# Kernel tuning notes

Measured on AMD Instinct MI355X. Metric: run time of the kernel, lower is better.

Reference implementation:

```python
import jax, jax.numpy as jnp
import numpy as np

B, S, D = 1, 4096, 2048
H, KV, HD = 16, 4, 128
GROUPS = H // KV
SCALE = HD ** -0.5
ROPE_BASE = 10000.0
NEG = -1e9


def _rope_tables():
    inv_freq = 1.0 / (ROPE_BASE ** (jnp.arange(0, HD, 2, dtype=jnp.float32) / HD))  # [HD/2]
    pos = jnp.arange(S, dtype=jnp.float32)
    freqs = pos[:, None] * inv_freq[None, :]            # [S, HD/2]
    emb = jnp.concatenate([freqs, freqs], axis=-1)      # [S, HD] (HF convention)
    return jnp.cos(emb)[None], jnp.sin(emb)[None]       # [1, S, HD]


def setup_inputs() -> dict:
    key = jax.random.key(0)
    ks = jax.random.split(key, 6)
    cos, sin = _rope_tables()
    causal = jnp.tril(jnp.ones((S, S), dtype=bool))
    attention_mask = jnp.where(causal, 0.0, NEG).astype(jnp.float32)[None, None]  # [1,1,S,S]
    std = 0.02
    return {
        "hidden_states": jax.random.normal(ks[0], (B, S, D), jnp.float32),
        "cos": cos.astype(jnp.float32),
        "sin": sin.astype(jnp.float32),
        "attention_mask": attention_mask,
        "wq": jax.random.normal(ks[1], (H * HD, D), jnp.float32) * std,
        "wk": jax.random.normal(ks[2], (KV * HD, D), jnp.float32) * std,
        "wv": jax.random.normal(ks[3], (KV * HD, D), jnp.float32) * std,
        "wo": jax.random.normal(ks[4], (D, H * HD), jnp.float32) * std,
    }


def _rotate_half(x):
    x1, x2 = x[..., : HD // 2], x[..., HD // 2:]
    return jnp.concatenate([-x2, x1], axis=-1)


def reference(hidden_states, cos, sin, attention_mask, wq, wk, wv, wo):
    b, s, _ = hidden_states.shape
    # projections -> [B, n_heads, S, HD]
    q = (hidden_states @ wq.T).reshape(b, s, H, HD).transpose(0, 2, 1, 3)
    k = (hidden_states @ wk.T).reshape(b, s, KV, HD).transpose(0, 2, 1, 3)
    v = (hidden_states @ wv.T).reshape(b, s, KV, HD).transpose(0, 2, 1, 3)
    # RoPE (HF apply_rotary_pos_emb, unsqueeze head dim)
    c, sn = cos[:, None], sin[:, None]
    q = q * c + _rotate_half(q) * sn
    k = k * c + _rotate_half(k) * sn
    # GQA: repeat kv heads
    k = jnp.repeat(k, GROUPS, axis=1)
    v = jnp.repeat(v, GROUPS, axis=1)
    # eager attention
    scores = jnp.einsum("bhqd,bhkd->bhqk", q, k) * SCALE + attention_mask
    attn = jax.nn.softmax(scores, axis=-1)
    out = jnp.einsum("bhqk,bhkd->bhqd", attn, v)
    out = out.transpose(0, 2, 1, 3).reshape(b, s, H * HD)
    # output projection (all-reduce is identity at world_size=1)
    return out @ wo.T
```

## Files before the change

kernel.cpp:

```cpp
#include <hip/hip_runtime.h>
#include <hip/hip_bf16.h>

#define SEQ   4096
#define DMODEL 2048
#define NHEAD 16
#define NKVH  4
#define HDIM  128
#define NQ    (NHEAD*HDIM)
#define NKV   (NKVH*HDIM)
#define NQKV  (NQ + 2*NKV)
#define SCALE 0.08838834764831845f
#define LOG2E 1.4426950408889634f
#define SCL2  (SCALE * LOG2E)

typedef __bf16 bf16x4 __attribute__((ext_vector_type(4)));
typedef __bf16 bf16x8 __attribute__((ext_vector_type(8)));
typedef float  f32x4  __attribute__((ext_vector_type(4)));

#define GLOBAL_CPTR(x) ((const __attribute__((address_space(1))) void*)(x))
#define LDS_PTR(x)     ((__attribute__((address_space(3))) void*)(x))

__global__ __launch_bounds__(256)
void convert_kernel(__bf16* __restrict__ dst, const float* __restrict__ src, int n8)
{
    const int i = blockIdx.x * 256 + threadIdx.x;
    if (i >= n8) return;
    const size_t e0 = (size_t)i * 8;
    const float4 a = *(const float4*)(src + e0);
    const float4 b = *(const float4*)(src + e0 + 4);
    bf16x8 o;
    o[0]=(__bf16)a.x; o[1]=(__bf16)a.y; o[2]=(__bf16)a.z; o[3]=(__bf16)a.w;
    o[4]=(__bf16)b.x; o[5]=(__bf16)b.y; o[6]=(__bf16)b.z; o[7]=(__bf16)b.w;
    *(bf16x8*)(dst + e0) = o;
}

__global__ __launch_bounds__(256)
void gemm_bt(const __bf16* __restrict__ A, const __bf16* __restrict__ Bw,
             void* __restrict__ Cv, __bf16* __restrict__ kb2, __bf16* __restrict__ vt2,
             const float* __restrict__ ct, const float* __restrict__ st,
             int M, int N, int K, int cmode)
{
    __shared__ alignas(16) __bf16 As[2][128*32];
    __shared__ alignas(16) __bf16 Bs[2][128*32];

    const int tid  = threadIdx.x;
    const int w    = tid >> 6;
    const int lane = tid & 63;
    const int l16  = lane & 15;
    const int quad = lane >> 4;
    const int m0 = blockIdx.y * 128;
    const int n0 = blockIdx.x * 128;

    const int srow = lane >> 2;
    const int scol = (lane & 3) * 8;

    const int wm = (w >> 1) * 64;
    int coff[4];
    #pragma unroll
    for (int nt = 0; nt < 4; ++nt)
        coff[nt] = (cmode == 3) ? ((w & 1) * 32 + ((nt & 2) ? 64 : 0) + (nt & 1) * 16)
                                : ((w & 1) * 64 + nt * 16);

    f32x4 acc[4][4];
    #pragma unroll
    for (int mt = 0; mt < 4; ++mt)
        #pragma unroll
        for (int nt = 0; nt < 4; ++nt)
            acc[mt][nt] = (f32x4){0.f, 0.f, 0.f, 0.f};

    auto STAGE = [&](int k0, int b) {
        #pragma unroll
        for (int c = 0; c < 2; ++c) {
            const int r0 = w * 32 + c * 16;
            const __bf16* ga = A + (size_t)(m0 + r0 + srow) * K + k0 + scol;
            __builtin_amdgcn_global_load_lds(GLOBAL_CPTR(ga), LDS_PTR(&As[b][r0 * 32]), 16, 0, 0);
            const __bf16* gb = Bw + (size_t)(n0 + r0 + srow) * K + k0 + scol;
            __builtin_amdgcn_global_load_lds(GLOBAL_CPTR(gb), LDS_PTR(&Bs[b][r0 * 32]), 16, 0, 0);
        }
    };

    STAGE(0, 0);
    for (int k0 = 0; k0 < K; k0 += 32) {
        const int b = (k0 >> 5) & 1;
        __syncthreads();
        if (k0 + 32 < K) STAGE(k0 + 32, b ^ 1);

        bf16x8 af[4], bf[4];
        #pragma unroll
        for (int mt = 0; mt < 4; ++mt)
            af[mt] = *(const bf16x8*)&As[b][(wm + mt*16 + l16) * 32 + quad * 8];
        #pragma unroll
        for (int nt = 0; nt < 4; ++nt)
            bf[nt] = *(const bf16x8*)&Bs[b][(coff[nt] + l16) * 32 + quad * 8];
        __builtin_amdgcn_s_setprio(1);
        #pragma unroll
        for (int mt = 0; mt < 4; ++mt)
            #pragma unroll
            for (int nt = 0; nt < 4; ++nt)
                acc[mt][nt] = __builtin_amdgcn_mfma_f32_16x16x32_bf16(
                    af[mt], bf[nt], acc[mt][nt], 0, 0, 0);
        __builtin_amdgcn_s_setprio(0);
    }

    if (cmode == 3) {
        if (n0 >= 2560) {
            #pragma unroll
            for (int mt = 0; mt < 4; ++mt)
                #pragma unroll
                for (int nt = 0; nt < 4; ++nt) {
                    const int col = (n0 - 2560) + coff[nt] + l16;
                    const int row = m0 + wm + mt*16 + quad*4;
                    bf16x4 pk;
                    #pragma unroll
                    for (int r = 0; r < 4; ++r) pk[r] = (__bf16)acc[mt][nt][r];
                    *(bf16x4*)&vt2[(size_t)col * M + row] = pk;
                }
        } else {
            __bf16* dst;
            int ncols, cb;
            if (n0 < 2048) { dst = (__bf16*)Cv; ncols = NQ;  cb = n0; }
            else           { dst = kb2;         ncols = NKV; cb = n0 - 2048; }
            #pragma unroll
            for (int mt = 0; mt < 4; ++mt)
                #pragma unroll
                for (int np = 0; np < 2; ++np) {
                    const int d = coff[np] + l16;
                    #pragma unroll
                    for (int r = 0; r < 4; ++r) {
                        const int s = m0 + wm + mt*16 + quad*4 + r;
                        const float c  = ct[s * HDIM + d];
                        const float sn = st[s * HDIM + d];
                        const float x1 = acc[mt][np][r];
                        const float x2 = acc[mt][np + 2][r];
                        dst[(size_t)s * ncols + cb + d]      = (__bf16)(x1 * c - x2 * sn);
                        dst[(size_t)s * ncols + cb + d + 64] = (__bf16)(x2 * c + x1 * sn);
                    }
                }
        }
    } else if (cmode == 1) {
        float* Cf = (float*)Cv;
        #pragma unroll
        for (int mt = 0; mt < 4; ++mt)
            #pragma unroll
            for (int nt = 0; nt < 4; ++nt) {
                const int row = m0 + wm + mt*16 + quad*4;
                const int col = n0 + coff[nt] + l16;
                #pragma unroll
                for (int r = 0; r < 4; ++r)
                    Cf[(size_t)(row + r) * N + col] = acc[mt][nt][r];
            }
    } else {
        __bf16* Cb = (__bf16*)Cv;
        #pragma unroll
        for (int mt = 0; mt < 4; ++mt)
            #pragma unroll
            for (int nt = 0; nt < 4; ++nt) {
                const int row = m0 + wm + mt*16 + quad*4;
                const int col = n0 + coff[nt] + l16;
                #pragma unroll
                for (int r = 0; r < 4; ++r)
                    Cb[(size_t)(row + r) * N + col] = (__bf16)acc[mt][nt][r];
            }
    }
}

__global__ __launch_bounds__(512, 4)
void attn_kernel(__bf16* __restrict__ QO, const __bf16* __restrict__ Kb,
                 const __bf16* __restrict__ Vt)
{
    __shared__ alignas(16) __bf16 Klds[2][4][64][32];
    __shared__ alignas(16) __bf16 Vlds[2][2][128][32];
    __shared__ alignas(16) __bf16 Ps[8][16][64];

    const int tid  = threadIdx.x;
    const int w    = tid >> 6;
    const int lane = tid & 63;
    const int l16  = lane & 15;
    const int quad = lane >> 4;
    const int bx = (int)blockIdx.x;
    const int h  = (int)blockIdx.y;
    const int g  = h >> 2;
    const int nbx = (int)gridDim.x;
    const int qt = (h < 8) ? (nbx - 1 - bx) : bx;
    const int m0 = qt * 128;
    const int wrow = m0 + w * 16;

    const int srow = lane >> 2;
    const int scol = (((lane & 3) ^ ((lane >> 3) & 3)) * 8);
    const int rsw  = (quad ^ ((l16 >> 1) & 3)) * 8;

    const int kcw = w & 3;
    const int hw  = w >> 2;

    bf16x8 qf[4];
    {
        const size_t qbase = (size_t)(wrow + l16) * NQ + h * HDIM;
        #pragma unroll
        for (int kc = 0; kc < 4; ++kc)
            qf[kc] = *(const bf16x8*)&QO[qbase + kc * 32 + quad * 8];
    }

    bf16x8 onesf;
    #pragma unroll
    for (int i = 0; i < 8; ++i) onesf[i] = (__bf16)1.0f;

    const __bf16* kSrc = Kb + (size_t)(hw * 32 + srow) * NKV + g * HDIM + kcw * 32 + scol;
    const __bf16* vSrc = Vt + (size_t)(g * HDIM + kcw * 32 + srow) * SEQ + hw * 32 + scol;

    auto STAGE = [&](int jj, int b) {
        const int n0g = jj * 64;
        #pragma unroll
        for (int c = 0; c < 2; ++c) {
            __builtin_amdgcn_global_load_lds(
                GLOBAL_CPTR(kSrc + (size_t)(n0g + c * 16) * NKV),
                LDS_PTR(&Klds[b][kcw][hw * 32 + c * 16][0]), 16, 0, 0);
            __builtin_amdgcn_global_load_lds(
                GLOBAL_CPTR(vSrc + (size_t)(c * 16) * SEQ + n0g),
                LDS_PTR(&Vlds[b][hw][kcw * 32 + c * 16][0]), 16, 0, 0);
        }
    };

    f32x4 lacc = (f32x4){0.f, 0.f, 0.f, 0.f};
    f32x4 oacc[8];
    #pragma unroll
    for (int t = 0; t < 8; ++t) oacc[t] = (f32x4){0.f, 0.f, 0.f, 0.f};

    const int njt = 2 * qt + 2;
    STAGE(0, 0);
    for (int j = 0; j < njt; ++j) {
        __syncthreads();
        if (j + 1 < njt) STAGE(j + 1, (j + 1) & 1);
        const int n0g = j * 64;
        if (n0g > wrow + 15) continue;
        const int b = j & 1;

        f32x4 sacc[4];
        #pragma unroll
        for (int nt = 0; nt < 4; ++nt) sacc[nt] = (f32x4){0.f, 0.f, 0.f, 0.f};
        __builtin_amdgcn_s_setprio(1);
        #pragma unroll
        for (int kc = 0; kc < 4; ++kc) {
            #pragma unroll
            for (int nt = 0; nt < 4; ++nt) {
                const bf16x8 kf = *(const bf16x8*)&Klds[b][kc][nt * 16 + l16][rsw];
                sacc[nt] = __builtin_amdgcn_mfma_f32_16x16x32_bf16(qf[kc], kf, sacc[nt], 0, 0, 0);
            }
        }
        __builtin_amdgcn_s_setprio(0);

        const bool needmask = (n0g + 64 > wrow);
        #pragma unroll
        for (int r = 0; r < 4; ++r) {
            const int qr = wrow + quad * 4 + r;
            const int prow = quad * 4 + r;
            const int pxor = (prow & 7) << 3;
            #pragma unroll
            for (int nt = 0; nt < 4; ++nt) {
                float e = exp2f(sacc[nt][r] * SCL2);
                if (needmask && (n0g + nt * 16 + l16) > qr) e = 0.f;
                Ps[w][prow][(nt * 16 + l16) ^ pxor] = (__bf16)e;
            }
        }

        bf16x8 pa[2];
        #pragma unroll
        for (int kc = 0; kc < 2; ++kc)
            pa[kc] = *(const bf16x8*)&Ps[w][l16][(kc * 32 + quad * 8) ^ ((l16 & 7) << 3)];

        __builtin_amdgcn_s_setprio(1);
        lacc = __builtin_amdgcn_mfma_f32_16x16x32_bf16(pa[0], onesf, lacc, 0, 0, 0);
        lacc = __builtin_amdgcn_mfma_f32_16x16x32_bf16(pa[1], onesf, lacc, 0, 0, 0);
        #pragma unroll
        for (int kc = 0; kc < 2; ++kc)
            #pragma unroll
            for (int t = 0; t < 8; ++t) {
                const bf16x8 vf = *(const bf16x8*)&Vlds[b][kc][t * 16 + l16][rsw];
                oacc[t] = __builtin_amdgcn_mfma_f32_16x16x32_bf16(pa[kc], vf, oacc[t], 0, 0, 0);
            }
        __builtin_amdgcn_s_setprio(0);
    }

    float rinv[4];
    #pragma unroll
    for (int r = 0; r < 4; ++r) rinv[r] = 1.f / lacc[r];
    #pragma unroll
    for (int t = 0; t < 8; ++t)
        #pragma unroll
        for (int r = 0; r < 4; ++r) {
            const int qr = wrow + quad * 4 + r;
            QO[(size_t)qr * NQ + h * HDIM + t * 16 + l16] = (__bf16)(oacc[t][r] * rinv[r]);
        }
}

extern "C" void kernel_launch(void* const* d_in, const int* in_sizes, int n_in,
                              void* d_out, int out_size, void* d_ws, size_t ws_size,
                              hipStream_t stream)
{
    const float* hidden = (const float*)d_in[0];
    const float* cosp   = (const float*)d_in[1];
    const float* sinp   = (const float*)d_in[2];
    const float* wq = (const float*)d_in[4];
    const float* wk = (const float*)d_in[5];
    const float* wv = (const float*)d_in[6];
    const float* wo = (const float*)d_in[7];

    const size_t nw_q = (size_t)NQ  * DMODEL;
    const size_t nw_k = (size_t)NKV * DMODEL;
    const size_t nq_e = (size_t)SEQ * NQ;
    const size_t nk_e = (size_t)SEQ * NKV;

    __bf16* ws     = (__bf16*)d_ws;
    __bf16* wo_b   = ws;
    __bf16* wqkv_b = wo_b + nw_q;
    __bf16* qbuf   = wqkv_b + nw_q + 2 * nw_k;
    __bf16* kbuf   = qbuf + nq_e;
    __bf16* vtb    = kbuf + nk_e;
    __bf16* hbuf   = (__bf16*)d_out;

    const dim3 blk(256);
    convert_kernel<<<dim3(nw_q / 8 / 256), blk, 0, stream>>>(wqkv_b, wq, nw_q / 8);
    convert_kernel<<<dim3(nw_k / 8 / 256), blk, 0, stream>>>(wqkv_b + nw_q, wk, nw_k / 8);
    convert_kernel<<<dim3(nw_k / 8 / 256), blk, 0, stream>>>(wqkv_b + nw_q + nw_k, wv, nw_k / 8);
    convert_kernel<<<dim3(nw_q / 8 / 256), blk, 0, stream>>>(wo_b, wo, nw_q / 8);
    convert_kernel<<<dim3(nq_e / 8 / 256), blk, 0, stream>>>(hbuf, hidden, nq_e / 8);

    gemm_bt<<<dim3(NQKV / 128, SEQ / 128), blk, 0, stream>>>(
        hbuf, wqkv_b, qbuf, kbuf, vtb, cosp, sinp, SEQ, NQKV, DMODEL, 3);

    attn_kernel<<<dim3(SEQ / 128, NHEAD), dim3(512), 0, stream>>>(qbuf, kbuf, vtb);

    gemm_bt<<<dim3(DMODEL / 128, SEQ / 128), blk, 0, stream>>>(
        qbuf, wo_b, d_out, nullptr, nullptr, nullptr, nullptr, SEQ, DMODEL, DMODEL, 1);
}
```

Measured before the change: 431.3 us.

## Rewrite GEMM with 256x256 tiles, XOR-swizzled LDS, and XCD-aware block remap

The projection GEMM moves from 128x128 tiles with 256 threads to 256x256 tiles with 512 threads and a K-step of 64. LDS staging now uses an XOR swizzle to avoid bank conflicts. A 1D grid is remapped so consecutive tiles land on the same XCD for L2 reuse. The main loop is split into four barrier-separated MFMA phases to overlap LDS reads with compute. The goals are more data reuse per tile and fewer LDS conflicts. In exchange, the 2048-wide output GEMM now launches only 128 blocks, which may underfill the 256 CUs, and register pressure rises with 128 accumulator floats per thread.

After: 447.0 us. 1.04x slower.

```diff
diff --git a/kernel.cpp b/kernel.cpp
--- a/kernel.cpp
+++ b/kernel.cpp
@@ -34,133 +34,201 @@
     *(bf16x8*)(dst + e0) = o;
 }
 
-__global__ __launch_bounds__(256)
+__global__ __launch_bounds__(512, 2)
 void gemm_bt(const __bf16* __restrict__ A, const __bf16* __restrict__ Bw,
              void* __restrict__ Cv, __bf16* __restrict__ kb2, __bf16* __restrict__ vt2,
              const float* __restrict__ ct, const float* __restrict__ st,
              int M, int N, int K, int cmode)
 {
-    __shared__ alignas(16) __bf16 As[2][128*32];
-    __shared__ alignas(16) __bf16 Bs[2][128*32];
+    __shared__ alignas(16) __bf16 As[2][256 * 64];
+    __shared__ alignas(16) __bf16 Bs[2][256 * 64];
 
     const int tid  = threadIdx.x;
     const int w    = tid >> 6;
     const int lane = tid & 63;
     const int l16  = lane & 15;
     const int quad = lane >> 4;
-    const int m0 = blockIdx.y * 128;
-    const int n0 = blockIdx.x * 128;
-
-    const int srow = lane >> 2;
-    const int scol = (lane & 3) * 8;
-
-    const int wm = (w >> 1) * 64;
-    int coff[4];
-    #pragma unroll
-    for (int nt = 0; nt < 4; ++nt)
-        coff[nt] = (cmode == 3) ? ((w & 1) * 32 + ((nt & 2) ? 64 : 0) + (nt & 1) * 16)
-                                : ((w & 1) * 64 + nt * 16);
-
-    f32x4 acc[4][4];
-    #pragma unroll
-    for (int mt = 0; mt < 4; ++mt)
-        #pragma unroll
-        for (int nt = 0; nt < 4; ++nt)
-            acc[mt][nt] = (f32x4){0.f, 0.f, 0.f, 0.f};
-
-    auto STAGE = [&](int k0, int b) {
-        #pragma unroll
-        for (int c = 0; c < 2; ++c) {
-            const int r0 = w * 32 + c * 16;
-            const __bf16* ga = A + (size_t)(m0 + r0 + srow) * K + k0 + scol;
-            __builtin_amdgcn_global_load_lds(GLOBAL_CPTR(ga), LDS_PTR(&As[b][r0 * 32]), 16, 0, 0);
-            const __bf16* gb = Bw + (size_t)(n0 + r0 + srow) * K + k0 + scol;
-            __builtin_amdgcn_global_load_lds(GLOBAL_CPTR(gb), LDS_PTR(&Bs[b][r0 * 32]), 16, 0, 0);
+    const int wr   = w >> 2;
+    const int wc   = w & 3;
+
+    const int nxt = N >> 8;
+    const int tot = nxt * (M >> 8);
+    const int bid = (int)blockIdx.x;
+    const int wg  = (bid & 7) * (tot >> 3) + (bid >> 3);
+    const int by  = wg / nxt;
+    const int bx2 = wg - by * nxt;
+    const int m0  = by << 8;
+    const int n0  = bx2 << 8;
+
+    int brow[2][2];
+    #pragma unroll
+    for (int nh = 0; nh < 2; ++nh)
+        #pragma unroll
+        for (int nt = 0; nt < 2; ++nt)
+            brow[nh][nt] = (cmode == 3)
+                ? ((wc >> 1) * 128 + (wc & 1) * 32 + nh * 64 + nt * 16)
+                : (wc * 64 + nh * 32 + nt * 16);
+
+    const int rr = lane >> 3;
+    const int ss = ((lane & 7) ^ rr) * 8;
+
+    f32x4 acc[8][4];
+    #pragma unroll
+    for (int mi = 0; mi < 8; ++mi)
+        #pragma unroll
+        for (int ni = 0; ni < 4; ++ni)
+            acc[mi][ni] = (f32x4){0.f, 0.f, 0.f, 0.f};
+
+    auto STAGE = [&](int k0, int p) {
+        #pragma unroll
+        for (int c = 0; c < 4; ++c) {
+            const int row = c * 64 + w * 8 + rr;
+            __builtin_amdgcn_global_load_lds(
+                GLOBAL_CPTR(A + (size_t)(m0 + row) * K + k0 + ss),
+                LDS_PTR(&As[p][c * 4096 + w * 512]), 16, 0, 0);
+            __builtin_amdgcn_global_load_lds(
+                GLOBAL_CPTR(Bw + (size_t)(n0 + row) * K + k0 + ss),
+                LDS_PTR(&Bs[p][c * 4096 + w * 512]), 16, 0, 0);
         }
     };
 
+    bf16x8 af[4][2], bfA[2][2], bfB[2][2];
+    const int xk = l16 & 7;
+
+    const int NT = K >> 6;
     STAGE(0, 0);
-    for (int k0 = 0; k0 < K; k0 += 32) {
-        const int b = (k0 >> 5) & 1;
-        __syncthreads();
-        if (k0 + 32 < K) STAGE(k0 + 32, b ^ 1);
-
-        bf16x8 af[4], bf[4];
-        #pragma unroll
-        for (int mt = 0; mt < 4; ++mt)
-            af[mt] = *(const bf16x8*)&As[b][(wm + mt*16 + l16) * 32 + quad * 8];
-        #pragma unroll
-        for (int nt = 0; nt < 4; ++nt)
-            bf[nt] = *(const bf16x8*)&Bs[b][(coff[nt] + l16) * 32 + quad * 8];
-        __builtin_amdgcn_s_setprio(1);
-        #pragma unroll
-        for (int mt = 0; mt < 4; ++mt)
-            #pragma unroll
-            for (int nt = 0; nt < 4; ++nt)
-                acc[mt][nt] = __builtin_amdgcn_mfma_f32_16x16x32_bf16(
-                    af[mt], bf[nt], acc[mt][nt], 0, 0, 0);
+    for (int t = 0; t < NT; ++t) {
+        const int p = t & 1;
+        asm volatile("s_waitcnt vmcnt(0)" ::: "memory");
+        __builtin_amdgcn_s_barrier();
+        __builtin_amdgcn_sched_barrier(0);
+        if (t + 1 < NT) STAGE((t + 1) << 6, p ^ 1);
+
+        #pragma unroll
+        for (int mt = 0; mt < 4; ++mt)
+            #pragma unroll
+            for (int kk = 0; kk < 2; ++kk)
+                af[mt][kk] = *(const bf16x8*)&As[p][(wr * 128 + mt * 16 + l16) * 64 + (((kk * 4 + quad) ^ xk) * 8)];
+        #pragma unroll
+        for (int nt = 0; nt < 2; ++nt)
+            #pragma unroll
+            for (int kk = 0; kk < 2; ++kk)
+                bfA[nt][kk] = *(const bf16x8*)&Bs[p][(brow[0][nt] + l16) * 64 + (((kk * 4 + quad) ^ xk) * 8)];
+        __builtin_amdgcn_s_barrier();
+        asm volatile("s_waitcnt lgkmcnt(0)" ::: "memory");
+        __builtin_amdgcn_sched_barrier(0);
+        __builtin_amdgcn_s_setprio(1);
+        #pragma unroll
+        for (int mt = 0; mt < 4; ++mt)
+            #pragma unroll
+            for (int nt = 0; nt < 2; ++nt)
+                #pragma unroll
+                for (int kk = 0; kk < 2; ++kk)
+                    acc[mt][nt] = __builtin_amdgcn_mfma_f32_16x16x32_bf16(af[mt][kk], bfA[nt][kk], acc[mt][nt], 0, 0, 0);
+        __builtin_amdgcn_s_setprio(0);
+        __builtin_amdgcn_s_barrier();
+
+        #pragma unroll
+        for (int nt = 0; nt < 2; ++nt)
+            #pragma unroll
+            for (int kk = 0; kk < 2; ++kk)
+                bfB[nt][kk] = *(const bf16x8*)&Bs[p][(brow[1][nt] + l16) * 64 + (((kk * 4 + quad) ^ xk) * 8)];
+        __builtin_amdgcn_s_barrier();
+        asm volatile("s_waitcnt lgkmcnt(0)" ::: "memory");
+        __builtin_amdgcn_sched_barrier(0);
+        __builtin_amdgcn_s_setprio(1);
+        #pragma unroll
+        for (int mt = 0; mt < 4; ++mt)
+            #pragma unroll
+            for (int nt = 0; nt < 2; ++nt)
+                #pragma unroll
+                for (int kk = 0; kk < 2; ++kk)
+                    acc[mt][2 + nt] = __builtin_amdgcn_mfma_f32_16x16x32_bf16(af[mt][kk], bfB[nt][kk], acc[mt][2 + nt], 0, 0, 0);
+        __builtin_amdgcn_s_setprio(0);
+        __builtin_amdgcn_s_barrier();
+
+        #pragma unroll
+        for (int mt = 0; mt < 4; ++mt)
+            #pragma unroll
+            for (int kk = 0; kk < 2; ++kk)
+                af[mt][kk] = *(const bf16x8*)&As[p][(wr * 128 + 64 + mt * 16 + l16) * 64 + (((kk * 4 + quad) ^ xk) * 8)];
+        __builtin_amdgcn_s_barrier();
+        asm volatile("s_waitcnt lgkmcnt(0)" ::: "memory");
+        __builtin_amdgcn_sched_barrier(0);
+        __builtin_amdgcn_s_setprio(1);
+        #pragma unroll
+        for (int mt = 0; mt < 4; ++mt)
+            #pragma unroll
+            for (int nt = 0; nt < 2; ++nt)
+                #pragma unroll
+                for (int kk = 0; kk < 2; ++kk)
+                    acc[4 + mt][2 + nt] = __builtin_amdgcn_mfma_f32_16x16x32_bf16(af[mt][kk], bfB[nt][kk], acc[4 + mt][2 + nt], 0, 0, 0);
+        __builtin_amdgcn_s_setprio(0);
+        __builtin_amdgcn_s_barrier();
+
+        __builtin_amdgcn_s_setprio(1);
+        #pragma unroll
+        for (int mt = 0; mt < 4; ++mt)
+            #pragma unroll
+            for (int nt = 0; nt < 2; ++nt)
+                #pragma unroll
+                for (int kk = 0; kk < 2; ++kk)
+                    acc[4 + mt][nt] = __builtin_amdgcn_mfma_f32_16x16x32_bf16(af[mt][kk], bfA[nt][kk], acc[4 + mt][nt], 0, 0, 0);
         __builtin_amdgcn_s_setprio(0);
     }
 
     if (cmode == 3) {
         if (n0 >= 2560) {
             #pragma unroll
-            for (int mt = 0; mt < 4; ++mt)
-                #pragma unroll
-                for (int nt = 0; nt < 4; ++nt) {
-                    const int col = (n0 - 2560) + coff[nt] + l16;
-                    const int row = m0 + wm + mt*16 + quad*4;
-                    bf16x4 pk;
+            for (int mi = 0; mi < 8; ++mi)
+                #pragma unroll
+                for (int nh = 0; nh < 2; ++nh)
                     #pragma unroll
-                    for (int r = 0; r < 4; ++r) pk[r] = (__bf16)acc[mt][nt][r];
-                    *(bf16x4*)&vt2[(size_t)col * M + row] = pk;
-                }
+                    for (int nt = 0; nt < 2; ++nt) {
+                        const int col = (n0 - 2560) + (wc >> 1) * 128 + (wc & 1) * 32 + nh * 64 + nt * 16 + l16;
+                        const int row0 = m0 + wr * 128 + mi * 16 + quad * 4;
+                        bf16x4 pk;
+                        #pragma unroll
+                        for (int r = 0; r < 4; ++r) pk[r] = (__bf16)acc[mi][nh * 2 + nt][r];
+                        *(bf16x4*)&vt2[(size_t)col * M + row0] = pk;
+                    }
         } else {
             __bf16* dst;
             int ncols, cb;
             if (n0 < 2048) { dst = (__bf16*)Cv; ncols = NQ;  cb = n0; }
             else           { dst = kb2;         ncols = NKV; cb = n0 - 2048; }
-            #pragma unroll
-            for (int mt = 0; mt < 4; ++mt)
-                #pragma unroll
-                for (int np = 0; np < 2; ++np) {
-                    const int d = coff[np] + l16;
+            const int hh = wc >> 1;
+            #pragma unroll
+            for (int mi = 0; mi < 8; ++mi)
+                #pragma unroll
+                for (int nt = 0; nt < 2; ++nt) {
+                    const int hloc = (wc & 1) * 32 + nt * 16 + l16;
                     #pragma unroll
                     for (int r = 0; r < 4; ++r) {
-                        const int s = m0 + wm + mt*16 + quad*4 + r;
-                        const float c  = ct[s * HDIM + d];
-                        const float sn = st[s * HDIM + d];
-                        const float x1 = acc[mt][np][r];
-                        const float x2 = acc[mt][np + 2][r];
-                        dst[(size_t)s * ncols + cb + d]      = (__bf16)(x1 * c - x2 * sn);
-                        dst[(size_t)s * ncols + cb + d + 64] = (__bf16)(x2 * c + x1 * sn);
+                        const int s = m0 + wr * 128 + mi * 16 + quad * 4 + r;
+                        const float c  = ct[s * HDIM + hloc];
+                        const float sn = st[s * HDIM + hloc];
+                        const float x1 = acc[mi][nt][r];
+                        const float x2 = acc[mi][2 + nt][r];
+                        dst[(size_t)s * ncols + cb + hh * 128 + hloc]      = (__bf16)(x1 * c - x2 * sn);
+                        dst[(size_t)s * ncols + cb + hh * 128 + hloc + 64] = (__bf16)(x2 * c + x1 * sn);
                     }
                 }
         }
-    } else if (cmode == 1) {
+    } else {
         float* Cf = (float*)Cv;
         #pragma unroll
-        for (int mt = 0; mt < 4; ++mt)
-            #pragma unroll
-            for (int nt = 0; nt < 4; ++nt) {
-                const int row = m0 + wm + mt*16 + quad*4;
-                const int col = n0 + coff[nt] + l16;
-                #pragma unroll
-                for (int r = 0; r < 4; ++r)
-                    Cf[(size_t)(row + r) * N + col] = acc[mt][nt][r];
-            }
-    } else {
-        __bf16* Cb = (__bf16*)Cv;
-        #pragma unroll
-        for (int mt = 0; mt < 4; ++mt)
-            #pragma unroll
-            for (int nt = 0; nt < 4; ++nt) {
-                const int row = m0 + wm + mt*16 + quad*4;
-                const int col = n0 + coff[nt] + l16;
-                #pragma unroll
-                for (int r = 0; r < 4; ++r)
-                    Cb[(size_t)(row + r) * N + col] = (__bf16)acc[mt][nt][r];
-            }
+        for (int mi = 0; mi < 8; ++mi)
+            #pragma unroll
+            for (int nh = 0; nh < 2; ++nh)
+                #pragma unroll
+                for (int nt = 0; nt < 2; ++nt) {
+                    const int row = m0 + wr * 128 + mi * 16 + quad * 4;
+                    const int col = n0 + wc * 64 + nh * 32 + nt * 16 + l16;
+                    #pragma unroll
+                    for (int r = 0; r < 4; ++r)
+                        Cf[(size_t)(row + r) * N + col] = acc[mi][nh * 2 + nt][r];
+                }
     }
 }
 
@@ -324,11 +392,11 @@
     convert_kernel<<<dim3(nw_q / 8 / 256), blk, 0, stream>>>(wo_b, wo, nw_q / 8);
     convert_kernel<<<dim3(nq_e / 8 / 256), blk, 0, stream>>>(hbuf, hidden, nq_e / 8);
 
-    gemm_bt<<<dim3(NQKV / 128, SEQ / 128), blk, 0, stream>>>(
+    gemm_bt<<<dim3((NQKV / 256) * (SEQ / 256)), dim3(512), 0, stream>>>(
         hbuf, wqkv_b, qbuf, kbuf, vtb, cosp, sinp, SEQ, NQKV, DMODEL, 3);
 
     attn_kernel<<<dim3(SEQ / 128, NHEAD), dim3(512), 0, stream>>>(qbuf, kbuf, vtb);
 
-    gemm_bt<<<dim3(DMODEL / 128, SEQ / 128), blk, 0, stream>>>(
+    gemm_bt<<<dim3((DMODEL / 256) * (SEQ / 256)), dim3(512), 0, stream>>>(
         qbuf, wo_b, d_out, nullptr, nullptr, nullptr, nullptr, SEQ, DMODEL, DMODEL, 1);
 }
```
